# Kernel tuning notes

Hardware: AMD Instinct MI355X
Metric: run time of the kernel (lower is better)

Reference implementation:

```python
import jax, jax.numpy as jnp
import numpy as np

LARGE = 1.0e6  # sentinel distance for 'no feature pixel found'
ALPHA, GAMMA = 0.25, 2.0
SMOOTH, LAMBDA = 1e-06, 1.0


def _col_dist(feat):
    # feat: [B,H,W] bool. Distance along axis 1 to nearest True at-or-before each row.
    H = feat.shape[1]
    i = jnp.arange(H, dtype=jnp.float32)[None, :, None]
    pos = jnp.where(feat, i, -LARGE)
    return i - jax.lax.cummax(pos, axis=1)


def _edt(feat):
    # Exact Euclidean distance transform: distance from every pixel to nearest True pixel.
    # Pass 1: 1-D distance along axis 1 (two directional scans via cummax).
    g = jnp.minimum(_col_dist(feat), jnp.flip(_col_dist(jnp.flip(feat, 1)), 1))
    g = jnp.minimum(g, LARGE)  # columns with no feature
    # Pass 2: d^2(i,j) = min_k g(i,k)^2 + (j-k)^2  (exact separable EDT)
    W = feat.shape[2]
    j = jnp.arange(W, dtype=jnp.float32)
    cost = (j[:, None] - j[None, :]) ** 2  # [W(j), W(k)]
    d2 = jnp.min(g[:, :, None, :] ** 2 + cost[None, None, :, :], axis=-1)  # [B,H,W]
    return jnp.sqrt(d2)


def _distance_weights(targets_f):
    # targets_f: [B,1,H,W] float 0/1 -> beta weights [B,1,H,W]
    m = targets_f[:, 0]  # [B,H,W]
    fg = _edt(m <= 0.5)  # dist of fg pixels to nearest bg (0 on bg) == scipy edt(m>0.5)
    bg = _edt(m > 0.5)   # dist of bg pixels to nearest fg (0 on fg) == scipy edt(m<=0.5)
    dist = jnp.where(m > 0.5, fg, -bg)
    max_dist = jnp.maximum(fg.max((1, 2)), bg.max((1, 2)))  # [B]
    has_fg = m.max((1, 2)) > 0
    valid = jnp.logical_and(has_fg, max_dist > 0)
    safe_md = jnp.maximum(max_dist, 1e-12)[:, None, None]
    w = 1.0 + jnp.exp(-jnp.abs(dist) / (safe_md / 3.0))
    w = jnp.where(valid[:, None, None], w, 1.0)
    return w[:, None]  # [B,1,H,W]


def _focal_loss(logits, t):
    p = jax.nn.sigmoid(logits)
    ce = -(t * jax.nn.log_sigmoid(logits) + (1.0 - t) * jax.nn.log_sigmoid(-logits))
    p_t = p * t + (1.0 - p) * (1.0 - t)
    focal_w = (1.0 - p_t) ** GAMMA
    alpha_t = ALPHA * t + (1.0 - ALPHA) * (1.0 - t)
    return jnp.mean(alpha_t * focal_w * ce)


def _iou_loss(logits, t, w):
    p = jax.nn.sigmoid(logits)
    inter = jnp.sum(p * t * w, axis=(2, 3))          # [B,1]
    union = jnp.sum((p + t) * w, axis=(2, 3)) - inter
    iou = (inter + SMOOTH) / (union + SMOOTH)
    return 1.0 - jnp.mean(iou)


def setup_inputs() -> dict:
    key = jax.random.key(0)
    ks = jax.random.split(key, 5)
    B, H, W = 8, 256, 256
    shp = (B, 1, H, W)
    return {
        "pred_main": jax.random.normal(ks[0], shp, jnp.float32),
        "aux0": jax.random.normal(ks[1], shp, jnp.float32),
        "aux1": jax.random.normal(ks[2], shp, jnp.float32),
        "aux2": jax.random.normal(ks[3], shp, jnp.float32),
        "targets": jax.random.randint(ks[4], shp, 0, 2).astype(jnp.int32),
    }


def reference(pred_main, aux0, aux1, aux2, targets):
    t = targets.astype(jnp.float32)
    beta = _distance_weights(t)
    total = LAMBDA * _focal_loss(pred_main, t) + _iou_loss(pred_main, t, beta)
    for i, aux in enumerate((aux0, aux1, aux2)):
        aux_loss = LAMBDA * _focal_loss(aux, t) + _iou_loss(aux, t, beta)
        total = total + (0.4 / (i + 1)) * aux_loss
    return total
```

## Files before the change

kernel.cpp:

```cpp
#include <hip/hip_runtime.h>
#include <math.h>

#define HH 256
#define WW 256
#define BB 8
#define NTOT (BB*HH*WW)
#define LARGE_F 1000000.0f
#define SCOPE __HIP_MEMORY_SCOPE_AGENT

typedef unsigned int u32;
typedef unsigned long long u64;


__device__ __forceinline__ float log_sigmoid_fast(float x) {
    return fminf(x, 0.0f) - __logf(1.0f + __expf(-fabsf(x)));
}

__device__ __forceinline__ void row_check(const u64* __restrict__ row,
                                          int k0, int r0, int c0, float dh2f,
                                          float* bestA, float* bestB) {
    u64 m0 = row[0], m1 = row[1], m2 = row[2], m3 = row[3];
    u64 n0 = ~m0, n1 = ~m1, n2 = ~m2, n3 = ~m3;

    int HbA = -1;
    if (k0 > 0 && m0) HbA = 63  - __builtin_clzll(m0);
    if (k0 > 1 && m1) HbA = 127 - __builtin_clzll(m1);
    if (k0 > 2 && m2) HbA = 191 - __builtin_clzll(m2);
    int RaA = 1 << 20;
    if (k0 < 3 && m3) RaA = 192 + __builtin_ctzll(m3);
    if (k0 < 2 && m2) RaA = 128 + __builtin_ctzll(m2);
    if (k0 < 1 && m1) RaA = 64  + __builtin_ctzll(m1);

    int HbB = -1;
    if (k0 > 0 && n0) HbB = 63  - __builtin_clzll(n0);
    if (k0 > 1 && n1) HbB = 127 - __builtin_clzll(n1);
    if (k0 > 2 && n2) HbB = 191 - __builtin_clzll(n2);
    int RaB = 1 << 20;
    if (k0 < 3 && n3) RaB = 192 + __builtin_ctzll(n3);
    if (k0 < 2 && n2) RaB = 128 + __builtin_ctzll(n2);
    if (k0 < 1 && n1) RaB = 64  + __builtin_ctzll(n1);

    u64 mk = (k0 == 0) ? m0 : (k0 == 1) ? m1 : (k0 == 2) ? m2 : m3;
    u64 nk = ~mk;
    const int base = 64 * k0;

    #pragma unroll
    for (int s = 0; s < 4; ++s) {
        int r = r0 + s, w = c0 + s;
        u64 le = (2ull << r) - 1ull;
        u64 ge = (~0ull) << r;
        {
            u64 lo = mk & le, hi = mk & ge;
            int L = lo ? (base + 63 - __builtin_clzll(lo)) : HbA;
            int R = hi ? (base + __builtin_ctzll(hi)) : RaA;
            int dl = (L >= 0) ? (w - L) : (1 << 20);
            int dr = R - w;
            float f = (float)min(dl, dr);
            bestA[s] = fminf(bestA[s], __builtin_fmaf(f, f, dh2f));
        }
        {
            u64 lo = nk & le, hi = nk & ge;
            int L = lo ? (base + 63 - __builtin_clzll(lo)) : HbB;
            int R = hi ? (base + __builtin_ctzll(hi)) : RaB;
            int dl = (L >= 0) ? (w - L) : (1 << 20);
            int dr = R - w;
            float f = (float)min(dl, dr);
            bestB[s] = fminf(bestB[s], __builtin_fmaf(f, f, dh2f));
        }
    }
}

__global__ void __launch_bounds__(256) k_fused(
    const float* __restrict__ p0, const float* __restrict__ p1,
    const float* __restrict__ p2, const float* __restrict__ p3,
    const int* __restrict__ tgt,
    u64* __restrict__ slabAB, float* __restrict__ partial,
    float* __restrict__ out)
{
    const int blk  = blockIdx.x;
    const int b    = blk >> 6;
    const int slab = blk & 63;
    const int wv   = threadIdx.x >> 6;
    const int lane = threadIdx.x & 63;
    const int h    = slab * 4 + wv;
    const int c0   = lane * 4;
    const int k0   = c0 >> 6;
    const int r0   = c0 & 63;
    const int rowbase = (b << 16) + (h << 8);

    __shared__ u64 sm[HH][4];
    __shared__ u64 sor[4], sand[4];
    __shared__ float wredA[4], wredB[4], smdv[2];
    __shared__ float red[4][12];
    __shared__ float fing[96];

    const int idx = rowbase + c0;
    float4 x40 = *(const float4*)(p0 + idx);
    float4 x41 = *(const float4*)(p1 + idx);
    float4 x42 = *(const float4*)(p2 + idx);
    float4 x43 = *(const float4*)(p3 + idx);

    {
        unsigned char* smb = (unsigned char*)&sm[0][0];
        const int tb = b << 16;
        #pragma unroll 4
        for (int it = 0; it < 32; ++it) {
            int P = it * 2048 + threadIdx.x * 8;
            int4 aa = *(const int4*)(tgt + tb + P);
            int4 cc = *(const int4*)(tgt + tb + P + 4);
            u32 by = (aa.x == 0 ? 1u : 0u) | (aa.y == 0 ? 2u : 0u) |
                     (aa.z == 0 ? 4u : 0u) | (aa.w == 0 ? 8u : 0u) |
                     (cc.x == 0 ? 16u : 0u) | (cc.y == 0 ? 32u : 0u) |
                     (cc.z == 0 ? 64u : 0u) | (cc.w == 0 ? 128u : 0u);
            smb[it * 256 + threadIdx.x] = (unsigned char)by;
        }
    }
    __syncthreads();

    {
        const int t = threadIdx.x;
        u64 w0 = sm[t][0], w1 = sm[t][1], w2 = sm[t][2], w3 = sm[t][3];
        u64 o = w0 | w1 | w2 | w3;
        u64 a = w0 & w1 & w2 & w3;
        #pragma unroll
        for (int off = 32; off > 0; off >>= 1) {
            o |= __shfl_down(o, off, 64);
            a &= __shfl_down(a, off, 64);
        }
        if (lane == 0) { sor[wv] = o; sand[wv] = a; }
    }
    __syncthreads();
    const u64 orAll  = sor[0] | sor[1] | sor[2] | sor[3];
    const u64 andAll = sand[0] & sand[1] & sand[2] & sand[3];
    const bool emptyA = (orAll == 0ull);
    const bool emptyB = (andAll == ~0ull);

    float bestA[4], bestB[4];
    #pragma unroll
    for (int s = 0; s < 4; ++s) {
        bestA[s] = emptyA ? 1.0f : 1e30f;
        bestB[s] = emptyB ? 1.0f : 1e30f;
    }
    row_check(&sm[h][0], k0, r0, c0, 0.0f, bestA, bestB);
    float bmax = 0.0f;
    #pragma unroll
    for (int s = 0; s < 4; ++s) bmax = fmaxf(bmax, fmaxf(bestA[s], bestB[s]));
    for (int dh = 1; dh < HH; ++dh) {
        float dh2f = (float)(dh * dh);
        if (dh2f >= bmax) break;
        int hd = h - dh, hu = h + dh;
        if (hd >= 0) row_check(&sm[hd][0], k0, r0, c0, dh2f, bestA, bestB);
        if (hu < HH) row_check(&sm[hu][0], k0, r0, c0, dh2f, bestA, bestB);
        bmax = 0.0f;
        #pragma unroll
        for (int s = 0; s < 4; ++s) bmax = fmaxf(bmax, fmaxf(bestA[s], bestB[s]));
    }

    const u64 mkown = sm[h][k0];
    float absd[4], tfv[4];
    float wmA = -1.0f, wmB = -1.0f;
    #pragma unroll
    for (int s = 0; s < 4; ++s) {
        float dA = emptyA ? LARGE_F : sqrtf(bestA[s]);
        float dB = emptyB ? LARGE_F : sqrtf(bestB[s]);
        wmA = fmaxf(wmA, dA);
        wmB = fmaxf(wmB, dB);
        int bit = (int)((mkown >> (r0 + s)) & 1ull);
        tfv[s]  = bit ? 0.0f : 1.0f;
        absd[s] = bit ? dB : dA;
    }
    #pragma unroll
    for (int off = 32; off > 0; off >>= 1) {
        wmA = fmaxf(wmA, __shfl_down(wmA, off, 64));
        wmB = fmaxf(wmB, __shfl_down(wmB, off, 64));
    }
    if (lane == 0) { wredA[wv] = wmA; wredB[wv] = wmB; }
    __syncthreads();
    if (threadIdx.x == 0) {
        float bA = fmaxf(fmaxf(wredA[0], wredA[1]), fmaxf(wredA[2], wredA[3]));
        float bB = fmaxf(fmaxf(wredB[0], wredB[1]), fmaxf(wredB[2], wredB[3]));
        u64 pk = ((u64)__float_as_uint(bB) << 32) | (u64)__float_as_uint(bA);
        __hip_atomic_store(&slabAB[blk], pk, __ATOMIC_RELAXED, SCOPE);
    }

    float vals[12];
    #pragma unroll
    for (int q = 0; q < 12; ++q) vals[q] = 0.0f;
    float pv[4][4];
    #pragma unroll
    for (int s = 0; s < 4; ++s) {
        float tf = tfv[s];
        #pragma unroll
        for (int i = 0; i < 4; ++i) {
            float x = (s == 0) ? ((i==0)?x40.x:(i==1)?x41.x:(i==2)?x42.x:x43.x)
                    : (s == 1) ? ((i==0)?x40.y:(i==1)?x41.y:(i==2)?x42.y:x43.y)
                    : (s == 2) ? ((i==0)?x40.z:(i==1)?x41.z:(i==2)?x42.z:x43.z)
                               : ((i==0)?x40.w:(i==1)?x41.w:(i==2)?x42.w:x43.w);
            float e = __expf(-x);
            float p = __builtin_amdgcn_rcpf(1.0f + e);
            float ce = -(tf * log_sigmoid_fast(x) + (1.0f - tf) * log_sigmoid_fast(-x));
            float p_t = p * tf + (1.0f - p) * (1.0f - tf);
            float om = 1.0f - p_t;
            float alpha_t = 0.25f * tf + 0.75f * (1.0f - tf);
            vals[i] += alpha_t * om * om * ce;
            pv[s][i] = p;
        }
    }

    if (wv == 0) {
        const int i = (b << 6) + lane;
        u64 v;
        for (;;) {
            v = __hip_atomic_load(&slabAB[i], __ATOMIC_RELAXED, SCOPE);
            if (!(v & 0x8000000080000000ull)) break;
            __builtin_amdgcn_s_sleep(1);
        }
        float a  = __uint_as_float((u32)v);
        float bb = __uint_as_float((u32)(v >> 32));
        #pragma unroll
        for (int off = 32; off > 0; off >>= 1) {
            a  = fmaxf(a,  __shfl_down(a,  off, 64));
            bb = fmaxf(bb, __shfl_down(bb, off, 64));
        }
        if (lane == 0) { smdv[0] = a; smdv[1] = bb; }
    }
    __syncthreads();
    const float md = fmaxf(smdv[0], smdv[1]);
    const bool valid = (!emptyB) && (md > 0.0f);
    const float inv = 3.0f / fmaxf(md, 1e-12f);

    #pragma unroll
    for (int s = 0; s < 4; ++s) {
        float wgt = valid ? (1.0f + __expf(-absd[s] * inv)) : 1.0f;
        float tf = tfv[s];
        #pragma unroll
        for (int i = 0; i < 4; ++i) {
            vals[4 + i] += tf * pv[s][i] * wgt;
            vals[8 + i] += (pv[s][i] + tf) * wgt;
        }
    }

    #pragma unroll
    for (int q = 0; q < 12; ++q) {
        float v = vals[q];
        #pragma unroll
        for (int o = 32; o > 0; o >>= 1) v += __shfl_down(v, o, 64);
        if (lane == 0) red[wv][q] = v;
    }
    __syncthreads();
    if (threadIdx.x < 12) {
        int q = threadIdx.x;
        float s = red[0][q] + red[1][q] + red[2][q] + red[3][q];
        __hip_atomic_store((u32*)&partial[blk * 12 + q], __float_as_uint(s),
                           __ATOMIC_RELAXED, SCOPE);
    }

    if (blk == 0) {
        if (threadIdx.x < 96) {
            const int bi = threadIdx.x / 12;
            const int qq = threadIdx.x % 12;
            float acc8[8];
            #pragma unroll
            for (int j = 0; j < 8; ++j) acc8[j] = 0.0f;
            for (int g8 = 0; g8 < 8; ++g8) {
                u32 raw[8];
                for (;;) {
                    bool bad = false;
                    #pragma unroll
                    for (int j = 0; j < 8; ++j)
                        raw[j] = __hip_atomic_load((u32*)&partial[((bi << 6) + g8 * 8 + j) * 12 + qq],
                                                   __ATOMIC_RELAXED, SCOPE);
                    #pragma unroll
                    for (int j = 0; j < 8; ++j) bad = bad || ((raw[j] >> 31) != 0u);
                    if (!bad) break;
                    __builtin_amdgcn_s_sleep(1);
                }
                #pragma unroll
                for (int j = 0; j < 8; ++j) acc8[j] += __uint_as_float(raw[j]);
            }
            fing[threadIdx.x] = ((acc8[0]+acc8[1])+(acc8[2]+acc8[3]))
                              + ((acc8[4]+acc8[5])+(acc8[6]+acc8[7]));
        }
        __syncthreads();
        if (threadIdx.x == 0) {
            const float coef[4] = {1.0f, 0.4f, 0.2f, 0.4f / 3.0f};
            float total = 0.0f;
            #pragma unroll
            for (int i = 0; i < 4; ++i) {
                float fm = 0.0f, ious = 0.0f;
                #pragma unroll
                for (int b2 = 0; b2 < BB; ++b2) {
                    fm += fing[b2 * 12 + i];
                    float in_ = fing[b2 * 12 + 4 + i];
                    float un  = fing[b2 * 12 + 8 + i] - in_;
                    ious += (in_ + 1e-6f) / (un + 1e-6f);
                }
                total += coef[i] * (fm / (float)NTOT + (1.0f - ious * 0.125f));
            }
            out[0] = total;
        }
    }
}

extern "C" void kernel_launch(void* const* d_in, const int* in_sizes, int n_in,
                              void* d_out, int out_size, void* d_ws, size_t ws_size,
                              hipStream_t stream) {
    const float* p0 = (const float*)d_in[0];
    const float* p1 = (const float*)d_in[1];
    const float* p2 = (const float*)d_in[2];
    const float* p3 = (const float*)d_in[3];
    const int* tgt = (const int*)d_in[4];
    float* out = (float*)d_out;

    char* w = (char*)d_ws;
    u64* slabAB    = (u64*)w;   w += 512 * sizeof(u64);
    float* partial = (float*)w; w += 512 * 12 * sizeof(float);

    k_fused<<<BB * 64, 256, 0, stream>>>(p0, p1, p2, p3, tgt, slabAB, partial, out);
}
```

Before: 89.73 us.

## Precompute target bitmask in separate kernel instead of per-block rebuild

Adds a small prepass kernel that converts the integer targets into per-row 64-bit ballot masks once, stored in workspace. The fused kernel then loads the compact mask for its batch image instead of every block re-reading and packing the full target image. This removes heavily redundant global/L2 reads. In exchange it adds a second launch and a serial dependency, and the prepass uses only 32 blocks.

```diff
diff --git a/kernel.cpp b/kernel.cpp
--- a/kernel.cpp
+++ b/kernel.cpp
@@ -14,6 +14,22 @@
 
 __device__ __forceinline__ float log_sigmoid_fast(float x) {
     return fminf(x, 0.0f) - __logf(1.0f + __expf(-fabsf(x)));
+}
+
+__global__ void __launch_bounds__(256) k_mask(const int* __restrict__ tgt,
+                                              u64* __restrict__ rowmask) {
+    const int b  = blockIdx.x >> 2;
+    const int hc = blockIdx.x & 3;
+    const int k  = threadIdx.x >> 6;
+    const int lane = threadIdx.x & 63;
+    const int colbase = (b << 16) + (k << 6) + lane;
+    #pragma unroll 4
+    for (int i = 0; i < 64; ++i) {
+        int h = (hc << 6) + i;
+        int tv = tgt[colbase + (h << 8)];
+        u64 bal = __ballot(tv == 0);
+        if (lane == 0) rowmask[(((b << 8) + h) << 2) + k] = bal;
+    }
 }
 
 __device__ __forceinline__ void row_check(const u64* __restrict__ row,
@@ -73,7 +89,7 @@
 __global__ void __launch_bounds__(256) k_fused(
     const float* __restrict__ p0, const float* __restrict__ p1,
     const float* __restrict__ p2, const float* __restrict__ p3,
-    const int* __restrict__ tgt,
+    const u64* __restrict__ rowmask,
     u64* __restrict__ slabAB, float* __restrict__ partial,
     float* __restrict__ out)
 {
@@ -100,26 +116,14 @@
     float4 x42 = *(const float4*)(p2 + idx);
     float4 x43 = *(const float4*)(p3 + idx);
 
-    {
-        unsigned char* smb = (unsigned char*)&sm[0][0];
-        const int tb = b << 16;
-        #pragma unroll 4
-        for (int it = 0; it < 32; ++it) {
-            int P = it * 2048 + threadIdx.x * 8;
-            int4 aa = *(const int4*)(tgt + tb + P);
-            int4 cc = *(const int4*)(tgt + tb + P + 4);
-            u32 by = (aa.x == 0 ? 1u : 0u) | (aa.y == 0 ? 2u : 0u) |
-                     (aa.z == 0 ? 4u : 0u) | (aa.w == 0 ? 8u : 0u) |
-                     (cc.x == 0 ? 16u : 0u) | (cc.y == 0 ? 32u : 0u) |
-                     (cc.z == 0 ? 64u : 0u) | (cc.w == 0 ? 128u : 0u);
-            smb[it * 256 + threadIdx.x] = (unsigned char)by;
-        }
-    }
-    __syncthreads();
-
+    u64 w0, w1, w2, w3;
     {
         const int t = threadIdx.x;
-        u64 w0 = sm[t][0], w1 = sm[t][1], w2 = sm[t][2], w3 = sm[t][3];
+        const u64* src = rowmask + (((b << 8) + t) << 2);
+        ulonglong2 v0 = *(const ulonglong2*)(src);
+        ulonglong2 v1 = *(const ulonglong2*)(src + 2);
+        w0 = v0.x; w1 = v0.y; w2 = v1.x; w3 = v1.y;
+        sm[t][0] = w0; sm[t][1] = w1; sm[t][2] = w2; sm[t][3] = w3;
         u64 o = w0 | w1 | w2 | w3;
         u64 a = w0 & w1 & w2 & w3;
         #pragma unroll
@@ -313,8 +317,10 @@
     float* out = (float*)d_out;
 
     char* w = (char*)d_ws;
+    u64* rowmask   = (u64*)w;   w += BB * HH * 4 * sizeof(u64);
     u64* slabAB    = (u64*)w;   w += 512 * sizeof(u64);
     float* partial = (float*)w; w += 512 * 12 * sizeof(float);
 
-    k_fused<<<BB * 64, 256, 0, stream>>>(p0, p1, p2, p3, tgt, slabAB, partial, out);
-}
+    k_mask<<<BB * 4, 256, 0, stream>>>(tgt, rowmask);
+    k_fused<<<BB * 64, 256, 0, stream>>>(p0, p1, p2, p3, rowmask, slabAB, partial, out);
+}
```

After: 100.7 us. 12.2% more time.

## Build target bitmask rows lazily per wave with ballot instead of full image

Applied to the files above, without the earlier changes.

Each block now builds only a small window of target bitmask rows around its slab with wave ballots, and loads further rows on demand as the distance search expands. This drops the full 256-row target read, the OR/AND emptiness reduction and one barrier per block. Emptiness is now inferred from unfound distances. The search loop now uses a wave-wide max as its stop condition, so divergence is uniform per wave. Concurrent per-wave writes of on-demand rows to shared memory without a barrier could race between waves, and sparse targets would fall back to serial row loads.

```diff
diff --git a/kernel.cpp b/kernel.cpp
--- a/kernel.cpp
+++ b/kernel.cpp
@@ -14,6 +14,23 @@
 
 __device__ __forceinline__ float log_sigmoid_fast(float x) {
     return fminf(x, 0.0f) - __logf(1.0f + __expf(-fabsf(x)));
+}
+
+__device__ __forceinline__ float wave_max(float v) {
+    #pragma unroll
+    for (int off = 32; off > 0; off >>= 1)
+        v = fmaxf(v, __shfl_xor(v, off, 64));
+    return v;
+}
+
+__device__ __forceinline__ void build_row(const int* __restrict__ tgt, int tb,
+                                          int row, int lane, u64 (*sm)[4]) {
+    const int base = tb + (row << 8) + lane;
+    u64 w0 = __ballot(tgt[base]       == 0);
+    u64 w1 = __ballot(tgt[base + 64]  == 0);
+    u64 w2 = __ballot(tgt[base + 128] == 0);
+    u64 w3 = __ballot(tgt[base + 192] == 0);
+    if (lane == 0) { sm[row][0] = w0; sm[row][1] = w1; sm[row][2] = w2; sm[row][3] = w3; }
 }
 
 __device__ __forceinline__ void row_check(const u64* __restrict__ row,
@@ -86,10 +103,10 @@
     const int c0   = lane * 4;
     const int k0   = c0 >> 6;
     const int r0   = c0 & 63;
-    const int rowbase = (b << 16) + (h << 8);
+    const int tb   = b << 16;
+    const int rowbase = tb + (h << 8);
 
     __shared__ u64 sm[HH][4];
-    __shared__ u64 sor[4], sand[4];
     __shared__ float wredA[4], wredB[4], smdv[2];
     __shared__ float red[4][12];
     __shared__ float fing[96];
@@ -100,69 +117,51 @@
     float4 x42 = *(const float4*)(p2 + idx);
     float4 x43 = *(const float4*)(p3 + idx);
 
-    {
-        unsigned char* smb = (unsigned char*)&sm[0][0];
-        const int tb = b << 16;
-        #pragma unroll 4
-        for (int it = 0; it < 32; ++it) {
-            int P = it * 2048 + threadIdx.x * 8;
-            int4 aa = *(const int4*)(tgt + tb + P);
-            int4 cc = *(const int4*)(tgt + tb + P + 4);
-            u32 by = (aa.x == 0 ? 1u : 0u) | (aa.y == 0 ? 2u : 0u) |
-                     (aa.z == 0 ? 4u : 0u) | (aa.w == 0 ? 8u : 0u) |
-                     (cc.x == 0 ? 16u : 0u) | (cc.y == 0 ? 32u : 0u) |
-                     (cc.z == 0 ? 64u : 0u) | (cc.w == 0 ? 128u : 0u);
-            smb[it * 256 + threadIdx.x] = (unsigned char)by;
-        }
+    const int lo0 = slab * 4 - 12;
+    #pragma unroll
+    for (int j = 0; j < 7; ++j) {
+        int row = lo0 + wv * 7 + j;
+        if (row >= 0 && row < HH) build_row(tgt, tb, row, lane, sm);
     }
     __syncthreads();
-
-    {
-        const int t = threadIdx.x;
-        u64 w0 = sm[t][0], w1 = sm[t][1], w2 = sm[t][2], w3 = sm[t][3];
-        u64 o = w0 | w1 | w2 | w3;
-        u64 a = w0 & w1 & w2 & w3;
-        #pragma unroll
-        for (int off = 32; off > 0; off >>= 1) {
-            o |= __shfl_down(o, off, 64);
-            a &= __shfl_down(a, off, 64);
-        }
-        if (lane == 0) { sor[wv] = o; sand[wv] = a; }
-    }
-    __syncthreads();
-    const u64 orAll  = sor[0] | sor[1] | sor[2] | sor[3];
-    const u64 andAll = sand[0] & sand[1] & sand[2] & sand[3];
-    const bool emptyA = (orAll == 0ull);
-    const bool emptyB = (andAll == ~0ull);
-
-    float bestA[4], bestB[4];
-    #pragma unroll
-    for (int s = 0; s < 4; ++s) {
-        bestA[s] = emptyA ? 1.0f : 1e30f;
-        bestB[s] = emptyB ? 1.0f : 1e30f;
-    }
+    int winLo = max(lo0, 0);
+    int winHi = min(lo0 + 27, HH - 1);
+
+    float bestA[4] = {1e30f, 1e30f, 1e30f, 1e30f};
+    float bestB[4] = {1e30f, 1e30f, 1e30f, 1e30f};
+
     row_check(&sm[h][0], k0, r0, c0, 0.0f, bestA, bestB);
     float bmax = 0.0f;
     #pragma unroll
     for (int s = 0; s < 4; ++s) bmax = fmaxf(bmax, fmaxf(bestA[s], bestB[s]));
+    float wbmax = wave_max(bmax);
+
     for (int dh = 1; dh < HH; ++dh) {
         float dh2f = (float)(dh * dh);
-        if (dh2f >= bmax) break;
+        if (dh2f >= wbmax) break;
         int hd = h - dh, hu = h + dh;
-        if (hd >= 0) row_check(&sm[hd][0], k0, r0, c0, dh2f, bestA, bestB);
-        if (hu < HH) row_check(&sm[hu][0], k0, r0, c0, dh2f, bestA, bestB);
+        if (hd >= 0) {
+            if (hd < winLo) { build_row(tgt, tb, hd, lane, sm); winLo = hd; }
+            row_check(&sm[hd][0], k0, r0, c0, dh2f, bestA, bestB);
+        }
+        if (hu < HH) {
+            if (hu > winHi) { build_row(tgt, tb, hu, lane, sm); winHi = hu; }
+            row_check(&sm[hu][0], k0, r0, c0, dh2f, bestA, bestB);
+        }
         bmax = 0.0f;
         #pragma unroll
         for (int s = 0; s < 4; ++s) bmax = fmaxf(bmax, fmaxf(bestA[s], bestB[s]));
-    }
-
+        wbmax = wave_max(bmax);
+    }
+
+    const bool emptyB = (bestB[0] >= 1e29f);
     const u64 mkown = sm[h][k0];
     float absd[4], tfv[4];
     float wmA = -1.0f, wmB = -1.0f;
     #pragma unroll
     for (int s = 0; s < 4; ++s) {
-        float dA = emptyA ? LARGE_F : sqrtf(bestA[s]);
-        float dB = emptyB ? LARGE_F : sqrtf(bestB[s]);
+        float dA = (bestA[s] >= 1e29f) ? LARGE_F : sqrtf(bestA[s]);
+        float dB = (bestB[s] >= 1e29f) ? LARGE_F : sqrtf(bestB[s]);
         wmA = fmaxf(wmA, dA);
         wmB = fmaxf(wmB, dB);
         int bit = (int)((mkown >> (r0 + s)) & 1ull);
```

Result: faster. 87.80 us (-2.1%).
